# Kernel optimization log

Hardware: AMD Instinct MI355X
Metric: run time of the kernel (lower is better)

## Reference

```python
import jax, jax.numpy as jnp
import numpy as np

I, H, O, B, T = 128, 64, 128, 512, 512  # input_dim, hidden, output, batch, max_seqlen


def _gru_scan(x, mask, Wih, Whh, bih, bhh):
    """Masked unidirectional GRU over padded batch. x:[B,T,I], mask:[B,T]."""
    Hd = Whh.shape[1]
    gx = jnp.einsum('bti,gi->btg', x, Wih) + bih  # [B,T,3H]

    def step(h, inp):
        gx_t, m_t = inp
        gh = h @ Whh.T + bhh
        r = jax.nn.sigmoid(gx_t[:, :Hd] + gh[:, :Hd])
        z = jax.nn.sigmoid(gx_t[:, Hd:2 * Hd] + gh[:, Hd:2 * Hd])
        n = jnp.tanh(gx_t[:, 2 * Hd:] + r * gh[:, 2 * Hd:])
        h_new = (1.0 - z) * n + z * h
        h = jnp.where(m_t[:, None], h_new, h)  # freeze state past seq end (packed-seq semantics)
        return h, h

    h0 = jnp.zeros((x.shape[0], Hd), x.dtype)
    _, hs = jax.lax.scan(step, h0, (gx.transpose(1, 0, 2), mask.T))
    return hs.transpose(1, 0, 2)  # [B,T,H]


def setup_inputs():
    rng = np.random.default_rng(0)
    seqlens_np = rng.integers(1, T + 1, size=B)
    total = int(seqlens_np.sum())
    seqlens = jnp.asarray(seqlens_np, dtype=jnp.int32)
    key = jax.random.key(0)
    ks = jax.random.split(key, 12)
    s = float(1.0 / np.sqrt(H))
    u = lambda k, sh: jax.random.uniform(k, sh, jnp.float32, -s, s)
    return dict(
        sequences=jax.random.normal(ks[0], (total, I), jnp.float32),
        seqlens=seqlens,
        Wih_f=u(ks[1], (3 * H, I)), Whh_f=u(ks[2], (3 * H, H)),
        bih_f=u(ks[3], (3 * H,)), bhh_f=u(ks[4], (3 * H,)),
        Wih_b=u(ks[5], (3 * H, I)), Whh_b=u(ks[6], (3 * H, H)),
        bih_b=u(ks[7], (3 * H,)), bhh_b=u(ks[8], (3 * H,)),
        Wm=u(ks[9], (O, 2 * H)), bm=u(ks[10], (O,)),
        ctx=jax.random.normal(ks[11], (O,), jnp.float32) * 0.1,
    )


def reference(sequences, seqlens, Wih_f, Whh_f, bih_f, bhh_f,
              Wih_b, Whh_b, bih_b, bhh_b, Wm, bm, ctx):
    total = sequences.shape[0]
    # ragged -> padded [B,T,I]
    offsets = jnp.cumsum(seqlens)
    starts = offsets - seqlens
    tok = jnp.arange(total)
    bid = jnp.searchsorted(offsets, tok, side='right')
    pos = tok - starts[bid]
    padded = jnp.zeros((B, T, I), sequences.dtype).at[bid, pos].set(sequences)
    t_idx = jnp.arange(T)
    mask = t_idx[None, :] < seqlens[:, None]  # [B,T]

    # bidirectional GRU (backward dir = reverse within valid length, scan, reverse back)
    out_f = _gru_scan(padded, mask, Wih_f, Whh_f, bih_f, bhh_f)
    rev = jnp.where(mask, seqlens[:, None] - 1 - t_idx[None, :], t_idx[None, :])
    x_rev = jnp.take_along_axis(padded, rev[:, :, None], axis=1)
    out_b = jnp.take_along_axis(
        _gru_scan(x_rev, mask, Wih_b, Whh_b, bih_b, bhh_b), rev[:, :, None], axis=1)
    gru_out = jnp.concatenate([out_f, out_b], axis=-1)  # [B,T,2H]

    # MLP + tanh, then masked attention pooling with learned context vector
    mlp_out = jnp.tanh(jnp.einsum('btg,og->bto', gru_out, Wm) + bm)  # [B,T,O]
    scores = jnp.where(mask, mlp_out @ ctx, -1e9)
    w = jax.nn.softmax(scores, axis=1)  # [B,T]
    return jnp.einsum('bt,bto->bo', w, mlp_out)  # [B,O]
```

## Files before the change

kernel.cpp:

```cpp
#include <hip/hip_runtime.h>
#include <hip/hip_bf16.h>
#include <stdint.h>


typedef __attribute__((ext_vector_type(8))) short short8;
typedef __attribute__((ext_vector_type(4))) float f32x4;

__device__ __forceinline__ unsigned short f2bf(float f) {
  unsigned int u = __float_as_uint(f);
  u = (u + 0x7FFFu + ((u >> 16) & 1u)) >> 16;
  return (unsigned short)u;
}
__device__ __forceinline__ float bf2f(unsigned short h) {
  return __uint_as_float(((unsigned int)h) << 16);
}
__device__ __forceinline__ void f2bf2(float f, unsigned short& hi, unsigned short& lo) {
  hi = f2bf(f);
  lo = f2bf(f - bf2f(hi));
}
__device__ __forceinline__ f32x4 mfma16(short8 a, short8 b, f32x4 c) {
  return __builtin_amdgcn_mfma_f32_16x16x32_bf16(a, b, c, 0, 0, 0);
}
__device__ __forceinline__ float rcpf(float x) { return __builtin_amdgcn_rcpf(x); }
__device__ __forceinline__ float sigm(float x) { return rcpf(1.f + __expf(-x)); }
__device__ __forceinline__ float tanhft(float x) {
  float e = __expf(2.f * x);
  return 1.f - 2.f * rcpf(e + 1.f);
}

__global__ void k_offsets(const int* __restrict__ seqlens, int* __restrict__ off) {
  __shared__ int s[512];
  int t = threadIdx.x;
  s[t] = seqlens[t];
  __syncthreads();
  for (int d = 1; d < 512; d <<= 1) {
    int v = (t >= d) ? s[t - d] : 0;
    __syncthreads();
    s[t] += v;
    __syncthreads();
  }
  if (t == 0) off[0] = 0;
  off[t + 1] = s[t];
}

__global__ void k_prep(const float* __restrict__ Wih_f, const float* __restrict__ Wih_b,
                       const float* __restrict__ bih_f, const float* __restrict__ bhh_f,
                       const float* __restrict__ bih_b, const float* __restrict__ bhh_b,
                       const float* __restrict__ Wm,
                       unsigned short* __restrict__ Wcat_hi, unsigned short* __restrict__ Wcat_lo,
                       float* __restrict__ biasA,
                       unsigned short* __restrict__ Wm_hi, unsigned short* __restrict__ Wm_lo) {
  int idx = blockIdx.x * 256 + threadIdx.x;
  int stride = gridDim.x * 256;
  for (int i = idx; i < 384 * 128; i += stride) {
    int r = i >> 7, c = i & 127;
    float v = (r < 192) ? Wih_f[r * 128 + c] : Wih_b[(r - 192) * 128 + c];
    unsigned short hi, lo;
    f2bf2(v, hi, lo);
    Wcat_hi[i] = hi;
    Wcat_lo[i] = lo;
  }
  for (int i = idx; i < 128 * 128; i += stride) {
    unsigned short hi, lo;
    f2bf2(Wm[i], hi, lo);
    Wm_hi[i] = hi;
    Wm_lo[i] = lo;
  }
  for (int i = idx; i < 384; i += stride) {
    int d = i / 192, j = i % 192;
    const float* bi = d ? bih_b : bih_f;
    const float* bh = d ? bhh_b : bhh_f;
    biasA[i] = bi[j] + ((j < 128) ? bh[j] : 0.f);
  }
}

__global__ __launch_bounds__(256) void k_gemm_gx(
    const float* __restrict__ x, const unsigned short* __restrict__ Bhi,
    const unsigned short* __restrict__ Blo, const float* __restrict__ biasA,
    float* __restrict__ gx, int total) {
  __shared__ unsigned short Ahi[64][136];
  __shared__ unsigned short Alo[64][136];
  const int tid = threadIdx.x;
  const int base = blockIdx.x * 64;
  {
    int row = tid & 63, cc = tid >> 6;
    int grow = base + row;
    if (grow >= total) grow = total - 1;
    const float* src = x + (size_t)grow * 128 + cc * 32;
#pragma unroll
    for (int u = 0; u < 8; ++u) {
      f32x4 v = *(const f32x4*)(src + u * 4);
#pragma unroll
      for (int e = 0; e < 4; ++e) {
        unsigned short h_, l_;
        f2bf2(v[e], h_, l_);
        Ahi[row][cc * 32 + u * 4 + e] = h_;
        Alo[row][cc * 32 + u * 4 + e] = l_;
      }
    }
  }
  __syncthreads();
  const int w = tid >> 6, l = tid & 63;
  const int lr = l & 15, lg = l >> 4;
  short8 afh[4], afl[4];
#pragma unroll
  for (int kc = 0; kc < 4; ++kc) {
    afh[kc] = *(const short8*)&Ahi[w * 16 + lr][kc * 32 + lg * 8];
    afl[kc] = *(const short8*)&Alo[w * 16 + lr][kc * 32 + lg * 8];
  }
#pragma unroll 1
  for (int nt = 0; nt < 24; ++nt) {
    const int ncol = nt * 16 + lr;
    const float bias = biasA[ncol];
    f32x4 acc = {bias, bias, bias, bias};
#pragma unroll
    for (int kc = 0; kc < 4; ++kc) {
      short8 bh = *(const short8*)(Bhi + (size_t)ncol * 128 + kc * 32 + lg * 8);
      short8 bl = *(const short8*)(Blo + (size_t)ncol * 128 + kc * 32 + lg * 8);
      acc = mfma16(afh[kc], bh, acc);
      acc = mfma16(afl[kc], bh, acc);
      acc = mfma16(afh[kc], bl, acc);
    }
#pragma unroll
    for (int q = 0; q < 4; ++q) {
      int row = base + w * 16 + lg * 4 + q;
      if (row < total) gx[(size_t)row * 384 + ncol] = acc[q];
    }
  }
}

__global__ __launch_bounds__(256, 1) void k_scan(
    const float* __restrict__ gx, const int* __restrict__ off,
    const int* __restrict__ seqlens, const float* __restrict__ Whh_f,
    const float* __restrict__ Whh_b, const float* __restrict__ bhh_f,
    const float* __restrict__ bhh_b, float* __restrict__ hs) {
  __shared__ unsigned short hbuf[2][2][2][16][40];
  const int wg = blockIdx.x;
  const int dir = wg & 1;
  const int sblk = wg >> 1;
  const int tid = threadIdx.x;
  const int w = tid >> 6, l = tid & 63;
  const int b16 = l & 15, lg = l >> 4;
  const int seq = sblk * 16 + b16;
  const int len = seqlens[seq];
  const int start = off[seq];
  const float* Whh = dir ? Whh_b : Whh_f;
  const float* bhh = dir ? bhh_b : bhh_f;
  const int dirbase = dir * 192;
  const int j0 = w * 16 + lg * 4;

  short8 Ah[3][2], Al[3][2];
#pragma unroll
  for (int g = 0; g < 3; ++g) {
#pragma unroll
    for (int kc = 0; kc < 2; ++kc) {
      const float* wp = Whh + (size_t)(g * 64 + w * 16 + b16) * 64 + kc * 32 + lg * 8;
      f32x4 v0 = *(const f32x4*)wp;
      f32x4 v1 = *(const f32x4*)(wp + 4);
      short8 hh, ll;
#pragma unroll
      for (int e = 0; e < 4; ++e) {
        unsigned short h_, l_;
        f2bf2(v0[e], h_, l_);
        hh[e] = (short)h_;
        ll[e] = (short)l_;
      }
#pragma unroll
      for (int e = 0; e < 4; ++e) {
        unsigned short h_, l_;
        f2bf2(v1[e], h_, l_);
        hh[4 + e] = (short)h_;
        ll[4 + e] = (short)l_;
      }
      Ah[g][kc] = hh;
      Al[g][kc] = ll;
    }
  }
  const f32x4 bhhN = *(const f32x4*)(bhh + 128 + j0);

  int ml = len;
#pragma unroll
  for (int m = 1; m < 16; m <<= 1) ml = max(ml, __shfl_xor(ml, m, 64));
  const int ml8 = (ml + 7) & ~7;

  const int kcW = w >> 1;
  const int koffW = (w & 1) * 16 + lg * 4;
  {
    uint2 z2;
    z2.x = 0u; z2.y = 0u;
    *(uint2*)&hbuf[0][0][kcW][b16][koffW] = z2;
    *(uint2*)&hbuf[0][1][kcW][b16][koffW] = z2;
  }
  f32x4 h = {0.f, 0.f, 0.f, 0.f};
  asm volatile("s_waitcnt lgkmcnt(0)" ::: "memory");
  __builtin_amdgcn_s_barrier();
  __builtin_amdgcn_sched_barrier(0);

  const int p0 = dir ? (len - 1) : 0;
  const float* gp = gx + (size_t)(start + p0) * 384 + dirbase + j0;
  float* hp = hs + (size_t)(start + p0) * 128 + dir * 64 + j0;
  const ptrdiff_t gstep = dir ? -384 : 384;
  const ptrdiff_t hstep = dir ? -128 : 128;

  f32x4 Gr[8], Gz[8], Gn[8];
#pragma unroll
  for (int i = 0; i < 8; ++i) {
    Gr[i] = *(const f32x4*)gp;
    Gz[i] = *(const f32x4*)(gp + 64);
    Gn[i] = *(const f32x4*)(gp + 128);
    if (i + 1 < len) gp += gstep;
  }

#define SCAN_STEP(K)                                                           \
  {                                                                            \
    const int s = t + (K);                                                     \
    short8 bhf0 = *(const short8*)&hbuf[(K) & 1][0][0][b16][lg * 8];           \
    short8 bhf1 = *(const short8*)&hbuf[(K) & 1][0][1][b16][lg * 8];           \
    short8 blf0 = *(const short8*)&hbuf[(K) & 1][1][0][b16][lg * 8];           \
    short8 blf1 = *(const short8*)&hbuf[(K) & 1][1][1][b16][lg * 8];           \
    f32x4 ara = Gr[K], aza = Gz[K], ana = bhhN;                                \
    f32x4 zz = {0.f, 0.f, 0.f, 0.f};                                           \
    f32x4 arb = zz, azb = zz, anb = zz;                                        \
    ara = mfma16(Ah[0][0], bhf0, ara);                                         \
    aza = mfma16(Ah[1][0], bhf0, aza);                                         \
    ana = mfma16(Ah[2][0], bhf0, ana);                                         \
    arb = mfma16(Ah[0][1], bhf1, arb);                                         \
    azb = mfma16(Ah[1][1], bhf1, azb);                                         \
    anb = mfma16(Ah[2][1], bhf1, anb);                                         \
    ara = mfma16(Ah[0][0], blf0, ara);                                         \
    aza = mfma16(Ah[1][0], blf0, aza);                                         \
    ana = mfma16(Ah[2][0], blf0, ana);                                         \
    arb = mfma16(Ah[0][1], blf1, arb);                                         \
    azb = mfma16(Ah[1][1], blf1, azb);                                         \
    anb = mfma16(Ah[2][1], blf1, anb);                                         \
    ara = mfma16(Al[0][0], bhf0, ara);                                         \
    aza = mfma16(Al[1][0], bhf0, aza);                                         \
    ana = mfma16(Al[2][0], bhf0, ana);                                         \
    arb = mfma16(Al[0][1], bhf1, arb);                                         \
    azb = mfma16(Al[1][1], bhf1, azb);                                         \
    anb = mfma16(Al[2][1], bhf1, anb);                                         \
    f32x4 gn = Gn[K];                                                          \
                        \
    Gr[K] = *(const f32x4*)gp;                                                 \
    Gz[K] = *(const f32x4*)(gp + 64);                                          \
    Gn[K] = *(const f32x4*)(gp + 128);                                         \
    if (s + 9 < len) gp += gstep;                                              \
    f32x4 ar = ara + arb, az = aza + azb, an = ana + anb;                      \
    f32x4 hn;                                                                  \
    _Pragma("unroll") for (int q = 0; q < 4; ++q) {                            \
      float r = sigm(ar[q]);                                                   \
      float z = sigm(az[q]);                                                   \
      float n = tanhft(gn[q] + r * an[q]);                                     \
      hn[q] = z * (h[q] - n) + n;                                              \
    }                                                                          \
    const bool valid = (s < len);                                              \
    _Pragma("unroll") for (int q = 0; q < 4; ++q) h[q] = valid ? hn[q] : h[q]; \
    *(f32x4*)hp = h;      \
    if (s + 1 < len) hp += hstep;                                              \
       \
    unsigned int b0 = __float_as_uint(h[0]);                                   \
    unsigned int b1 = __float_as_uint(h[1]);                                   \
    unsigned int b2 = __float_as_uint(h[2]);                                   \
    unsigned int b3 = __float_as_uint(h[3]);                                   \
    uint2 whi;                                                                 \
    whi.x = (b0 >> 16) | (b1 & 0xFFFF0000u);                                   \
    whi.y = (b2 >> 16) | (b3 & 0xFFFF0000u);                                   \
    float l0 = h[0] - __uint_as_float(b0 & 0xFFFF0000u);                       \
    float l1 = h[1] - __uint_as_float(b1 & 0xFFFF0000u);                       \
    float l2 = h[2] - __uint_as_float(b2 & 0xFFFF0000u);                       \
    float l3 = h[3] - __uint_as_float(b3 & 0xFFFF0000u);                       \
    uint2 wlo;                                                                 \
    wlo.x = (__float_as_uint(l0) >> 16) | (__float_as_uint(l1) & 0xFFFF0000u); \
    wlo.y = (__float_as_uint(l2) >> 16) | (__float_as_uint(l3) & 0xFFFF0000u); \
    *(uint2*)&hbuf[((K) + 1) & 1][0][kcW][b16][koffW] = whi;                   \
    *(uint2*)&hbuf[((K) + 1) & 1][1][kcW][b16][koffW] = wlo;                   \
    asm volatile("s_waitcnt lgkmcnt(0)" ::: "memory");                         \
    __builtin_amdgcn_s_barrier();                                              \
    __builtin_amdgcn_sched_barrier(0);                                         \
  }

#pragma unroll 1
  for (int t = 0; t < ml8; t += 8) {
    SCAN_STEP(0)
    SCAN_STEP(1)
    SCAN_STEP(2)
    SCAN_STEP(3)
    SCAN_STEP(4)
    SCAN_STEP(5)
    SCAN_STEP(6)
    SCAN_STEP(7)
  }
#undef SCAN_STEP
}

__global__ __launch_bounds__(256) void k_gemm_mlp(
    const float* __restrict__ hs, const unsigned short* __restrict__ Bhi,
    const unsigned short* __restrict__ Blo, const float* __restrict__ bm,
    const float* __restrict__ ctx, float* __restrict__ mlp,
    float* __restrict__ scores, int total) {
  __shared__ unsigned short Ahi[64][136];
  __shared__ unsigned short Alo[64][136];
  const int tid = threadIdx.x;
  const int base = blockIdx.x * 64;
  {
    int row = tid & 63, cc = tid >> 6;
    int grow = base + row;
    if (grow >= total) grow = total - 1;
    const float* src = hs + (size_t)grow * 128 + cc * 32;
#pragma unroll
    for (int u = 0; u < 8; ++u) {
      f32x4 v = *(const f32x4*)(src + u * 4);
#pragma unroll
      for (int e = 0; e < 4; ++e) {
        unsigned short h_, l_;
        f2bf2(v[e], h_, l_);
        Ahi[row][cc * 32 + u * 4 + e] = h_;
        Alo[row][cc * 32 + u * 4 + e] = l_;
      }
    }
  }
  __syncthreads();
  const int w = tid >> 6, l = tid & 63;
  const int lr = l & 15, lg = l >> 4;
  short8 afh[4], afl[4];
#pragma unroll
  for (int kc = 0; kc < 4; ++kc) {
    afh[kc] = *(const short8*)&Ahi[w * 16 + lr][kc * 32 + lg * 8];
    afl[kc] = *(const short8*)&Alo[w * 16 + lr][kc * 32 + lg * 8];
  }
  float sc0 = 0.f, sc1 = 0.f, sc2 = 0.f, sc3 = 0.f;
#pragma unroll 1
  for (int nt = 0; nt < 8; ++nt) {
    const int ncol = nt * 16 + lr;
    const float bias = bm[ncol];
    const float cv = ctx[ncol];
    f32x4 acc = {bias, bias, bias, bias};
#pragma unroll
    for (int kc = 0; kc < 4; ++kc) {
      short8 bh = *(const short8*)(Bhi + (size_t)ncol * 128 + kc * 32 + lg * 8);
      short8 bl = *(const short8*)(Blo + (size_t)ncol * 128 + kc * 32 + lg * 8);
      acc = mfma16(afh[kc], bh, acc);
      acc = mfma16(afl[kc], bh, acc);
      acc = mfma16(afh[kc], bl, acc);
    }
    const int r0 = base + w * 16 + lg * 4;
    float tv0 = tanhft(acc[0]);
    float tv1 = tanhft(acc[1]);
    float tv2 = tanhft(acc[2]);
    float tv3 = tanhft(acc[3]);
    if (r0 + 0 < total) mlp[(size_t)(r0 + 0) * 128 + ncol] = tv0;
    if (r0 + 1 < total) mlp[(size_t)(r0 + 1) * 128 + ncol] = tv1;
    if (r0 + 2 < total) mlp[(size_t)(r0 + 2) * 128 + ncol] = tv2;
    if (r0 + 3 < total) mlp[(size_t)(r0 + 3) * 128 + ncol] = tv3;
    sc0 += tv0 * cv;
    sc1 += tv1 * cv;
    sc2 += tv2 * cv;
    sc3 += tv3 * cv;
  }
#pragma unroll
  for (int m = 1; m < 16; m <<= 1) {
    sc0 += __shfl_xor(sc0, m, 64);
    sc1 += __shfl_xor(sc1, m, 64);
    sc2 += __shfl_xor(sc2, m, 64);
    sc3 += __shfl_xor(sc3, m, 64);
  }
  if (lr == 0) {
    const int r0 = base + w * 16 + lg * 4;
    if (r0 + 0 < total) scores[r0 + 0] = sc0;
    if (r0 + 1 < total) scores[r0 + 1] = sc1;
    if (r0 + 2 < total) scores[r0 + 2] = sc2;
    if (r0 + 3 < total) scores[r0 + 3] = sc3;
  }
}

__global__ __launch_bounds__(512) void k_pool(
    const float* __restrict__ scores, const float* __restrict__ mlp,
    const int* __restrict__ off, const int* __restrict__ seqlens,
    float* __restrict__ out) {
  const int s = blockIdx.x;
  const int tid = threadIdx.x;
  const int len = seqlens[s];
  const int st = off[s];
  const int col = tid & 127, slice = tid >> 7;
  float m = (tid < len) ? scores[st + tid] : -1e30f;
#pragma unroll
  for (int d = 1; d < 64; d <<= 1) m = fmaxf(m, __shfl_xor(m, d, 64));
  __shared__ float wmx[8];
  if ((tid & 63) == 0) wmx[tid >> 6] = m;
  __syncthreads();
  m = wmx[0];
#pragma unroll
  for (int i = 1; i < 8; ++i) m = fmaxf(m, wmx[i]);
  float acc = 0.f, ws = 0.f;
  for (int t = slice; t < len; t += 4) {
    float wv = __expf(scores[st + t] - m);
    ws += wv;
    acc += wv * mlp[(size_t)(st + t) * 128 + col];
  }
  __shared__ float accs[4][128];
  __shared__ float wss[4];
  accs[slice][col] = acc;
  if (col == 0) wss[slice] = ws;
  __syncthreads();
  if (tid < 128) {
    float a = accs[0][tid] + accs[1][tid] + accs[2][tid] + accs[3][tid];
    float wsum = wss[0] + wss[1] + wss[2] + wss[3];
    out[(size_t)s * 128 + tid] = a * rcpf(wsum);
  }
}

extern "C" void kernel_launch(void* const* d_in, const int* in_sizes, int n_in,
                              void* d_out, int out_size, void* d_ws, size_t ws_size,
                              hipStream_t stream) {
  const float* seqs = (const float*)d_in[0];
  const int* seqlens = (const int*)d_in[1];
  const float* Wih_f = (const float*)d_in[2];
  const float* Whh_f = (const float*)d_in[3];
  const float* bih_f = (const float*)d_in[4];
  const float* bhh_f = (const float*)d_in[5];
  const float* Wih_b = (const float*)d_in[6];
  const float* Whh_b = (const float*)d_in[7];
  const float* bih_b = (const float*)d_in[8];
  const float* bhh_b = (const float*)d_in[9];
  const float* Wm = (const float*)d_in[10];
  const float* bm = (const float*)d_in[11];
  const float* ctx = (const float*)d_in[12];

  const int total = in_sizes[0] / 128;

  char* ws = (char*)d_ws;
  size_t o = 0;
  auto alloc = [&](size_t bytes) {
    size_t r = o;
    o = (o + bytes + 255) & ~(size_t)255;
    return r;
  };
  int* off = (int*)(ws + alloc(513 * 4));
  unsigned short* Wcat_hi = (unsigned short*)(ws + alloc(384 * 128 * 2));
  unsigned short* Wcat_lo = (unsigned short*)(ws + alloc(384 * 128 * 2));
  float* biasA = (float*)(ws + alloc(384 * 4));
  unsigned short* Wm_hi = (unsigned short*)(ws + alloc(128 * 128 * 2));
  unsigned short* Wm_lo = (unsigned short*)(ws + alloc(128 * 128 * 2));
  float* scores = (float*)(ws + alloc((size_t)total * 4));
  float* gxbuf = (float*)(ws + alloc((size_t)total * 384 * 4));
  float* hsbuf = (float*)(ws + alloc((size_t)total * 128 * 4));
  float* mlp = gxbuf;

  k_offsets<<<1, 512, 0, stream>>>(seqlens, off);
  k_prep<<<64, 256, 0, stream>>>(Wih_f, Wih_b, bih_f, bhh_f, bih_b, bhh_b, Wm,
                                 Wcat_hi, Wcat_lo, biasA, Wm_hi, Wm_lo);
  const int mt = (total + 63) / 64;
  k_gemm_gx<<<mt, 256, 0, stream>>>(seqs, Wcat_hi, Wcat_lo, biasA, gxbuf, total);
  k_scan<<<64, 256, 0, stream>>>(gxbuf, off, seqlens, Whh_f, Whh_b, bhh_f, bhh_b, hsbuf);
  k_gemm_mlp<<<mt, 256, 0, stream>>>(hsbuf, Wm_hi, Wm_lo, bm, ctx, mlp, scores, total);
  k_pool<<<512, 512, 0, stream>>>(scores, mlp, off, seqlens, (float*)d_out);
}
```

Baseline: 657.8 us.

## Stream scan gate inputs through double-buffered LDS via async global_load_lds

The GRU scan kernel no longer prefetches precomputed input-gate values eight steps ahead into registers. It now uses asynchronous global-to-LDS loads into a double-buffered shared array in chunks of four timesteps, and each step reads its gate values from LDS. The goal is to free many vector registers and hide global-load latency on the serial recurrence critical path. In exchange it adds LDS traffic and a vmcnt wait plus a barrier per chunk, and it relies on a non-trivial mapping between the load layout and the read layout.

```diff
diff --git a/kernel.cpp b/kernel.cpp
--- a/kernel.cpp
+++ b/kernel.cpp
@@ -27,6 +27,11 @@
   float e = __expf(2.f * x);
   return 1.f - 2.f * rcpf(e + 1.f);
 }
+
+#define GLDS(SRC, DST)                                        \
+  __builtin_amdgcn_global_load_lds(                           \
+      (const __attribute__((address_space(1))) void*)(SRC),   \
+      (__attribute__((address_space(3))) void*)(DST), 16, 0, 0)
 
 __global__ void k_offsets(const int* __restrict__ seqlens, int* __restrict__ off) {
   __shared__ int s[512];
@@ -134,6 +139,7 @@
     const int* __restrict__ seqlens, const float* __restrict__ Whh_f,
     const float* __restrict__ Whh_b, const float* __restrict__ bhh_f,
     const float* __restrict__ bhh_b, float* __restrict__ hs) {
+  __shared__ float gxl[2][4][3072];
   __shared__ unsigned short hbuf[2][2][2][16][40];
   const int wg = blockIdx.x;
   const int dir = wg & 1;
@@ -181,7 +187,7 @@
   int ml = len;
 #pragma unroll
   for (int m = 1; m < 16; m <<= 1) ml = max(ml, __shfl_xor(ml, m, 64));
-  const int ml8 = (ml + 7) & ~7;
+  const int ml4 = (ml + 3) & ~3;
 
   const int kcW = w >> 1;
   const int koffW = (w & 1) * 16 + lg * 4;
@@ -192,33 +198,36 @@
     *(uint2*)&hbuf[0][1][kcW][b16][koffW] = z2;
   }
   f32x4 h = {0.f, 0.f, 0.f, 0.f};
-  asm volatile("s_waitcnt lgkmcnt(0)" ::: "memory");
-  __builtin_amdgcn_s_barrier();
-  __builtin_amdgcn_sched_barrier(0);
 
   const int p0 = dir ? (len - 1) : 0;
-  const float* gp = gx + (size_t)(start + p0) * 384 + dirbase + j0;
+  const float* pp = gx + (size_t)(start + p0) * 384 + dirbase + lg * 4;
   float* hp = hs + (size_t)(start + p0) * 128 + dir * 64 + j0;
   const ptrdiff_t gstep = dir ? -384 : 384;
   const ptrdiff_t hstep = dir ? -128 : 128;
-
-  f32x4 Gr[8], Gz[8], Gn[8];
-#pragma unroll
-  for (int i = 0; i < 8; ++i) {
-    Gr[i] = *(const f32x4*)gp;
-    Gz[i] = *(const f32x4*)(gp + 64);
-    Gn[i] = *(const f32x4*)(gp + 128);
-    if (i + 1 < len) gp += gstep;
-  }
-
-#define SCAN_STEP(K)                                                           \
+  const int wcol = w * 48;
+
+  int tp = 0;
+#pragma unroll
+  for (int sc = 0; sc < 4; ++sc) {
+    GLDS(pp + wcol, &gxl[0][sc][(w * 3 + 0) * 256]);
+    GLDS(pp + wcol + 16, &gxl[0][sc][(w * 3 + 1) * 256]);
+    GLDS(pp + wcol + 32, &gxl[0][sc][(w * 3 + 2) * 256]);
+    if (tp + 1 < len) pp += gstep;
+    ++tp;
+  }
+
+#define SCAN_STEP(SC)                                                          \
   {                                                                            \
-    const int s = t + (K);                                                     \
-    short8 bhf0 = *(const short8*)&hbuf[(K) & 1][0][0][b16][lg * 8];           \
-    short8 bhf1 = *(const short8*)&hbuf[(K) & 1][0][1][b16][lg * 8];           \
-    short8 blf0 = *(const short8*)&hbuf[(K) & 1][1][0][b16][lg * 8];           \
-    short8 blf1 = *(const short8*)&hbuf[(K) & 1][1][1][b16][lg * 8];           \
-    f32x4 ara = Gr[K], aza = Gz[K], ana = bhhN;                                \
+    const int s = t0 + (SC);                                                   \
+    const float* gbase = &gxl[bf][SC][(w * 4 + lg) * 64 + b16 * 4];            \
+    f32x4 gxr = *(const f32x4*)gbase;                                          \
+    f32x4 gxz = *(const f32x4*)(gbase + 1024);                                 \
+    f32x4 gxn = *(const f32x4*)(gbase + 2048);                                 \
+    short8 bhf0 = *(const short8*)&hbuf[(SC) & 1][0][0][b16][lg * 8];          \
+    short8 bhf1 = *(const short8*)&hbuf[(SC) & 1][0][1][b16][lg * 8];          \
+    short8 blf0 = *(const short8*)&hbuf[(SC) & 1][1][0][b16][lg * 8];          \
+    short8 blf1 = *(const short8*)&hbuf[(SC) & 1][1][1][b16][lg * 8];          \
+    f32x4 ara = gxr, aza = gxz, ana = bhhN;                                    \
     f32x4 zz = {0.f, 0.f, 0.f, 0.f};                                           \
     f32x4 arb = zz, azb = zz, anb = zz;                                        \
     ara = mfma16(Ah[0][0], bhf0, ara);                                         \
@@ -239,25 +248,18 @@
     arb = mfma16(Al[0][1], bhf1, arb);                                         \
     azb = mfma16(Al[1][1], bhf1, azb);                                         \
     anb = mfma16(Al[2][1], bhf1, anb);                                         \
-    f32x4 gn = Gn[K];                                                          \
-                        \
-    Gr[K] = *(const f32x4*)gp;                                                 \
-    Gz[K] = *(const f32x4*)(gp + 64);                                          \
-    Gn[K] = *(const f32x4*)(gp + 128);                                         \
-    if (s + 9 < len) gp += gstep;                                              \
     f32x4 ar = ara + arb, az = aza + azb, an = ana + anb;                      \
     f32x4 hn;                                                                  \
     _Pragma("unroll") for (int q = 0; q < 4; ++q) {                            \
       float r = sigm(ar[q]);                                                   \
       float z = sigm(az[q]);                                                   \
-      float n = tanhft(gn[q] + r * an[q]);                                     \
+      float n = tanhft(gxn[q] + r * an[q]);                                    \
       hn[q] = z * (h[q] - n) + n;                                              \
     }                                                                          \
     const bool valid = (s < len);                                              \
     _Pragma("unroll") for (int q = 0; q < 4; ++q) h[q] = valid ? hn[q] : h[q]; \
     *(f32x4*)hp = h;      \
     if (s + 1 < len) hp += hstep;                                              \
-       \
     unsigned int b0 = __float_as_uint(h[0]);                                   \
     unsigned int b1 = __float_as_uint(h[1]);                                   \
     unsigned int b2 = __float_as_uint(h[2]);                                   \
@@ -272,25 +274,37 @@
     uint2 wlo;                                                                 \
     wlo.x = (__float_as_uint(l0) >> 16) | (__float_as_uint(l1) & 0xFFFF0000u); \
     wlo.y = (__float_as_uint(l2) >> 16) | (__float_as_uint(l3) & 0xFFFF0000u); \
-    *(uint2*)&hbuf[((K) + 1) & 1][0][kcW][b16][koffW] = whi;                   \
-    *(uint2*)&hbuf[((K) + 1) & 1][1][kcW][b16][koffW] = wlo;                   \
+    *(uint2*)&hbuf[((SC) + 1) & 1][0][kcW][b16][koffW] = whi;                  \
+    *(uint2*)&hbuf[((SC) + 1) & 1][1][kcW][b16][koffW] = wlo;                  \
     asm volatile("s_waitcnt lgkmcnt(0)" ::: "memory");                         \
     __builtin_amdgcn_s_barrier();                                              \
     __builtin_amdgcn_sched_barrier(0);                                         \
   }
 
 #pragma unroll 1
-  for (int t = 0; t < ml8; t += 8) {
+  for (int t0 = 0; t0 < ml4; t0 += 4) {
+    const int bf = (t0 >> 2) & 1;
+    const int bfn = bf ^ 1;
+    __builtin_amdgcn_sched_barrier(0);
+#pragma unroll
+    for (int sc = 0; sc < 4; ++sc) {
+      GLDS(pp + wcol, &gxl[bfn][sc][(w * 3 + 0) * 256]);
+      GLDS(pp + wcol + 16, &gxl[bfn][sc][(w * 3 + 1) * 256]);
+      GLDS(pp + wcol + 32, &gxl[bfn][sc][(w * 3 + 2) * 256]);
+      if (tp + 1 < len) pp += gstep;
+      ++tp;
+    }
+    __builtin_amdgcn_sched_barrier(0);
+    asm volatile("s_waitcnt vmcnt(12) lgkmcnt(0)" ::: "memory");
+    __builtin_amdgcn_s_barrier();
+    __builtin_amdgcn_sched_barrier(0);
     SCAN_STEP(0)
     SCAN_STEP(1)
     SCAN_STEP(2)
     SCAN_STEP(3)
-    SCAN_STEP(4)
-    SCAN_STEP(5)
-    SCAN_STEP(6)
-    SCAN_STEP(7)
   }
 #undef SCAN_STEP
+  asm volatile("s_waitcnt vmcnt(0)" ::: "memory");
 }
 
 __global__ __launch_bounds__(256) void k_gemm_mlp(
```

Result: slower. 847.9 us (+28.9%).
